# Performance work log

Hardware: AMD Instinct MI355X
Metric: run time of the kernel (lower is better)

## Reference

```python
import jax, jax.numpy as jnp
import numpy as np

N_GROUPS = 32
EPS = 1e-5
N_HEADS = 8
D_K = 64


def setup_inputs() -> dict:
    key = jax.random.key(0)
    ks = jax.random.split(key, 4)
    B, C, H, W = 16, 512, 32, 32
    x = jax.random.normal(ks[0], (B, C, H, W), dtype=jnp.float32)
    gn_w = jnp.ones((C,), dtype=jnp.float32)
    gn_b = jnp.zeros((C,), dtype=jnp.float32)
    proj_w = jax.random.normal(ks[1], (3 * C, C), dtype=jnp.float32) * (C ** -0.5)
    proj_b = jnp.zeros((3 * C,), dtype=jnp.float32)
    out_w = jax.random.normal(ks[2], (C, C), dtype=jnp.float32) * (C ** -0.5)
    out_b = jnp.zeros((C,), dtype=jnp.float32)
    return {"x": x, "gn_w": gn_w, "gn_b": gn_b, "proj_w": proj_w,
            "proj_b": proj_b, "out_w": out_w, "out_b": out_b}


def _group_norm(x, w, b):
    B, C, H, W = x.shape
    xg = x.reshape(B, N_GROUPS, C // N_GROUPS, H, W)
    mean = xg.mean(axis=(2, 3, 4), keepdims=True)
    var = xg.var(axis=(2, 3, 4), keepdims=True)
    xn = (xg - mean) * jax.lax.rsqrt(var + EPS)
    xn = xn.reshape(B, C, H, W)
    return xn * w[None, :, None, None] + b[None, :, None, None]


def reference(x, gn_w, gn_b, proj_w, proj_b, out_w, out_b):
    B, C, H, W = x.shape
    S = H * W
    scale = D_K ** -0.25  # applied to both q and k, as in the original
    h = _group_norm(x, gn_w, gn_b).reshape(B, C, S).transpose(0, 2, 1)  # [B,S,C]
    qkv = h @ proj_w.T + proj_b  # [B,S,3C]
    qkv = qkv.reshape(B, S, N_HEADS, 3 * D_K)
    q, k, v = jnp.split(qkv, 3, axis=-1)  # each [B,S,H,D]
    attn = jnp.einsum('bihd,bjhd->bijh', q * scale, k * scale)  # [B,S,S,Hd]
    attn = jax.nn.softmax(attn, axis=2)
    res = jnp.einsum('bijh,bjhd->bihd', attn, v).reshape(B, S, N_HEADS * D_K)
    res = res @ out_w.T + out_b  # [B,S,C]
    res = res.transpose(0, 2, 1).reshape(B, C, H, W)
    return res + x
```

## Files before the change

kernel.cpp:

```cpp
#include <hip/hip_runtime.h>
#include <stdint.h>

typedef unsigned short u16;
typedef __attribute__((ext_vector_type(8))) short bf16x8;
typedef __attribute__((ext_vector_type(4))) short bf16x4;
typedef __attribute__((ext_vector_type(4))) float f32x4;
typedef __attribute__((ext_vector_type(4))) unsigned short u16x4;

__device__ __forceinline__ u16 f2b(float f) {
  union { float f; unsigned u; } v; v.f = f;
  unsigned r = v.u + 0x7FFFu + ((v.u >> 16) & 1u);
  return (u16)(r >> 16);
}

__device__ __forceinline__ float fexp2(float x) {
#if __has_builtin(__builtin_amdgcn_exp2f)
  return __builtin_amdgcn_exp2f(x);
#else
  return exp2f(x);
#endif
}

__global__ __launch_bounds__(256) void cvt_kernel(const float* __restrict__ wq_f,
                                                  const float* __restrict__ wo_f,
                                                  u16* __restrict__ wq,
                                                  u16* __restrict__ wo) {
  int i = blockIdx.x * 256 + threadIdx.x;
  const float* src; u16* dst; int j;
  if (i < 196608) { src = wq_f; dst = wq; j = i; }
  else            { src = wo_f; dst = wo; j = i - 196608; }
  const float4 f = ((const float4*)src)[j];
  u16x4 r; r[0] = f2b(f.x); r[1] = f2b(f.y); r[2] = f2b(f.z); r[3] = f2b(f.w);
  *(u16x4*)(dst + (size_t)j * 4) = r;
}

__global__ __launch_bounds__(256) void gn_kernel(const float* __restrict__ x,
                                                 const float* __restrict__ gw,
                                                 const float* __restrict__ gb,
                                                 u16* __restrict__ h) {
  const int b = blockIdx.x >> 5, g = blockIdx.x & 31;
  const float* xg = x + ((size_t)(b * 512 + g * 16)) * 1024;
  const int tid = threadIdx.x;
  float vals[64];
  float s = 0.f, ss = 0.f;
#pragma unroll
  for (int i = 0; i < 64; i++) {
    float vv = xg[i * 256 + tid];
    vals[i] = vv; s += vv; ss += vv * vv;
  }
#pragma unroll
  for (int off = 32; off; off >>= 1) { s += __shfl_down(s, off); ss += __shfl_down(ss, off); }
  __shared__ float red[8];
  const int wid = tid >> 6, lane = tid & 63;
  if (lane == 0) { red[wid] = s; red[4 + wid] = ss; }
  __syncthreads();
  if (tid == 0) {
    float S = red[0] + red[1] + red[2] + red[3];
    float SS = red[4] + red[5] + red[6] + red[7];
    float mean = S * (1.f / 16384.f);
    float var = SS * (1.f / 16384.f) - mean * mean;
    red[0] = mean; red[1] = rsqrtf(var + 1e-5f);
  }
  __syncthreads();
  const float mean = red[0], rs = red[1];
  float sc[16], bi[16];
#pragma unroll
  for (int c = 0; c < 16; c++) { sc[c] = gw[g * 16 + c] * rs; bi[c] = gb[g * 16 + c]; }
#pragma unroll
  for (int h4 = 0; h4 < 4; h4++) {
    const int sp = h4 * 256 + tid;
    u16 row[16];
#pragma unroll
    for (int c = 0; c < 16; c++)
      row[c] = f2b((vals[c * 4 + h4] - mean) * sc[c] + bi[c]);
    u16* dst = h + ((size_t)(b * 1024 + sp)) * 512 + g * 16;
    *(bf16x8*)dst = *(bf16x8*)&row[0];
    *(bf16x8*)(dst + 8) = *(bf16x8*)&row[8];
  }
}

#define TSTRIDE 36

__global__ __launch_bounds__(256) void qkv_gemm(const u16* __restrict__ h,
                                                const u16* __restrict__ w,
                                                const float* __restrict__ bias,
                                                u16* __restrict__ q,
                                                u16* __restrict__ k,
                                                u16* __restrict__ v) {
  __shared__ u16 As[2][128 * TSTRIDE];
  __shared__ u16 Bs[2][128 * TSTRIDE];
  const int b = blockIdx.z;
  const int bm = blockIdx.x;
  const int bn = blockIdx.y;
  const int tid = threadIdx.x, lane = tid & 63, wid = tid >> 6;
  const int wm = wid & 1, wn = wid >> 1;
  const u16* gA = h + ((size_t)b * 1024 + bm * 128) * 512;
  const u16* gB = w + (size_t)bn * 128 * 512;

  const f32x4 fz = {0.f, 0.f, 0.f, 0.f};
  f32x4 acc[4][4];
#pragma unroll
  for (int i = 0; i < 4; i++)
#pragma unroll
    for (int j = 0; j < 4; j++) acc[i][j] = fz;

  int srow[2], soff[2];
#pragma unroll
  for (int j = 0; j < 2; j++) {
    srow[j] = (wid * 2 + j) * 16 + (lane >> 2);
    soff[j] = srow[j] * TSTRIDE + (lane & 3) * 8;
  }
  const int ch8 = (lane & 3) * 8;
  const int c15 = lane & 15, quad = lane >> 4;

  bf16x8 ar[2], br[2];
#pragma unroll
  for (int j = 0; j < 2; j++) {
    ar[j] = *(const bf16x8*)(gA + (size_t)srow[j] * 512 + ch8);
    br[j] = *(const bf16x8*)(gB + (size_t)srow[j] * 512 + ch8);
  }
#pragma unroll
  for (int j = 0; j < 2; j++) {
    *(bf16x8*)&As[0][soff[j]] = ar[j];
    *(bf16x8*)&Bs[0][soff[j]] = br[j];
  }
#pragma unroll
  for (int j = 0; j < 2; j++) {
    ar[j] = *(const bf16x8*)(gA + (size_t)srow[j] * 512 + 32 + ch8);
    br[j] = *(const bf16x8*)(gB + (size_t)srow[j] * 512 + 32 + ch8);
  }

  for (int kt = 0; kt < 16; ++kt) {
    __syncthreads();
    const int cur = kt & 1, alt = cur ^ 1;
    if (kt < 15) {
#pragma unroll
      for (int j = 0; j < 2; j++) {
        *(bf16x8*)&As[alt][soff[j]] = ar[j];
        *(bf16x8*)&Bs[alt][soff[j]] = br[j];
      }
      const int pk2 = (kt + 2) & 15;
#pragma unroll
      for (int j = 0; j < 2; j++) {
        ar[j] = *(const bf16x8*)(gA + (size_t)srow[j] * 512 + pk2 * 32 + ch8);
        br[j] = *(const bf16x8*)(gB + (size_t)srow[j] * 512 + pk2 * 32 + ch8);
      }
    }
    bf16x8 af[4], bf[4];
#pragma unroll
    for (int mi = 0; mi < 4; mi++)
      af[mi] = *(const bf16x8*)&As[cur][(wm * 64 + mi * 16 + c15) * TSTRIDE + quad * 8];
#pragma unroll
    for (int ni = 0; ni < 4; ni++)
      bf[ni] = *(const bf16x8*)&Bs[cur][(wn * 64 + ni * 16 + c15) * TSTRIDE + quad * 8];
#pragma unroll
    for (int mi = 0; mi < 4; mi++)
#pragma unroll
      for (int ni = 0; ni < 4; ni++)
        acc[mi][ni] = __builtin_amdgcn_mfma_f32_16x16x32_bf16(af[mi], bf[ni], acc[mi][ni], 0, 0, 0);
  }

  const float qscale = 0.51006972f;
  const float kscale = 0.35355339059327373f;
  const int quad4 = quad << 2;
#pragma unroll
  for (int mi = 0; mi < 4; mi++) {
    const int m = bm * 128 + wm * 64 + mi * 16 + quad4;
#pragma unroll
    for (int ni = 0; ni < 4; ni++) {
      const int n = bn * 128 + wn * 64 + ni * 16 + c15;
      const int head = n / 192;
      const int rr = n - head * 192;
      const float bi = bias[n];
      const int d = rr & 63;
      if (rr < 128) {
        u16* dst = (rr < 64) ? q : k;
        const float sc = (rr < 64) ? qscale : kscale;
        dst += ((size_t)(b * 8 + head) * 1024 + m) * 64 + d;
#pragma unroll
        for (int r = 0; r < 4; r++)
          dst[(size_t)r * 64] = f2b((acc[mi][ni][r] + bi) * sc);
      } else {
        u16x4 pk;
#pragma unroll
        for (int r = 0; r < 4; r++) pk[r] = f2b(acc[mi][ni][r] + bi);
        *(u16x4*)(v + ((size_t)(b * 8 + head) * 64 + d) * 1024 + m) = pk;
      }
    }
  }
}

__global__ __launch_bounds__(256) void attn_kernel(const u16* __restrict__ q,
                                                   const u16* __restrict__ k,
                                                   const u16* __restrict__ vT,
                                                   u16* __restrict__ o) {
  __shared__ u16 Ks[2][64 * 64];
  __shared__ u16 Vs[2][64 * 64];
  const int bh = blockIdx.x;
  const int qb = blockIdx.y;
  const int tid = threadIdx.x, lane = tid & 63, wid = tid >> 6;
  const u16* Q = q + (size_t)bh * 1024 * 64;
  const u16* K = k + (size_t)bh * 1024 * 64;
  const u16* V = vT + (size_t)bh * 64 * 1024;
  const int qrow0 = qb * 128 + wid * 32;
  const int c15 = lane & 15, quad = lane >> 4;
  const int sw = c15 & 7;
  const int srow = tid >> 2;
  const int t4 = tid & 3;
  const int s7 = srow & 7;
  const int kld0 = srow * 64 + (((t4 * 2) ^ s7) * 8);
  const int kld1 = srow * 64 + (((t4 * 2 + 1) ^ s7) * 8);
  int vld[4];
#pragma unroll
  for (int qq = 0; qq < 4; qq++)
    vld[qq] = srow * 64 + ((((t4 >> 1) * 4 + qq) ^ s7) * 8) + (t4 & 1) * 4;

  bf16x8 qf[2][2];
#pragma unroll
  for (int kk = 0; kk < 2; kk++)
#pragma unroll
    for (int ni = 0; ni < 2; ni++)
      qf[kk][ni] = *(const bf16x8*)(Q + (size_t)(qrow0 + ni * 16 + c15) * 64 + kk * 32 + quad * 8);

  const f32x4 fz = {0.f, 0.f, 0.f, 0.f};
  const float Mshift = 14.4269504089f;
  const f32x4 fm = {-Mshift, -Mshift, -Mshift, -Mshift};
  f32x4 oaccT[4][2];
#pragma unroll
  for (int i = 0; i < 4; i++)
#pragma unroll
    for (int j = 0; j < 2; j++) oaccT[i][j] = fz;
  float lsum[2] = {0.f, 0.f};

  bf16x8 kr0, kr1, vr0, vr1;
  {
    const u16* Kn = K + (size_t)srow * 64 + t4 * 16;
    kr0 = *(const bf16x8*)(Kn); kr1 = *(const bf16x8*)(Kn + 8);
    const u16* Vn = V + (size_t)srow * 1024 + t4 * 16;
    vr0 = *(const bf16x8*)(Vn); vr1 = *(const bf16x8*)(Vn + 8);
  }
  {
    u16* Kd = Ks[0]; u16* Vd = Vs[0];
    *(bf16x8*)&Kd[kld0] = kr0; *(bf16x8*)&Kd[kld1] = kr1;
    union { bf16x4 h[2]; bf16x8 v; } a0, a1;
    a0.v = vr0; a1.v = vr1;
    *(bf16x4*)&Vd[vld[0]] = a0.h[0];
    *(bf16x4*)&Vd[vld[1]] = a0.h[1];
    *(bf16x4*)&Vd[vld[2]] = a1.h[0];
    *(bf16x4*)&Vd[vld[3]] = a1.h[1];
  }
  {
    const u16* Kn = K + (size_t)(64 + srow) * 64 + t4 * 16;
    kr0 = *(const bf16x8*)(Kn); kr1 = *(const bf16x8*)(Kn + 8);
    const u16* Vn = V + (size_t)srow * 1024 + 64 + t4 * 16;
    vr0 = *(const bf16x8*)(Vn); vr1 = *(const bf16x8*)(Vn + 8);
  }

  for (int kt = 0; kt < 16; ++kt) {
    __syncthreads();
    const int cur = kt & 1, alt = cur ^ 1;
    if (kt < 15) {
      u16* Kd = Ks[alt]; u16* Vd = Vs[alt];
      *(bf16x8*)&Kd[kld0] = kr0; *(bf16x8*)&Kd[kld1] = kr1;
      union { bf16x4 h[2]; bf16x8 v; } a0, a1;
      a0.v = vr0; a1.v = vr1;
      *(bf16x4*)&Vd[vld[0]] = a0.h[0];
      *(bf16x4*)&Vd[vld[1]] = a0.h[1];
      *(bf16x4*)&Vd[vld[2]] = a1.h[0];
      *(bf16x4*)&Vd[vld[3]] = a1.h[1];
      const int pk2 = (kt + 2) & 15;
      const u16* Kn = K + ((size_t)pk2 * 64 + srow) * 64 + t4 * 16;
      kr0 = *(const bf16x8*)(Kn); kr1 = *(const bf16x8*)(Kn + 8);
      const u16* Vn = V + (size_t)srow * 1024 + pk2 * 64 + t4 * 16;
      vr0 = *(const bf16x8*)(Vn); vr1 = *(const bf16x8*)(Vn + 8);
    }
    const u16* Kc = Ks[cur];
    const u16* Vc = Vs[cur];

    f32x4 sacc[4][2];
#pragma unroll
    for (int i = 0; i < 4; i++)
#pragma unroll
      for (int j = 0; j < 2; j++) sacc[i][j] = fm;
#pragma unroll
    for (int kk = 0; kk < 2; kk++) {
      bf16x8 af[4];
#pragma unroll
      for (int mi = 0; mi < 4; mi++)
        af[mi] = *(const bf16x8*)&Kc[(mi * 16 + c15) * 64 + (((kk * 4 + quad) ^ sw) * 8)];
#pragma unroll
      for (int mi = 0; mi < 4; mi++)
#pragma unroll
        for (int ni = 0; ni < 2; ni++)
          sacc[mi][ni] = __builtin_amdgcn_mfma_f32_16x16x32_bf16(af[mi], qf[kk][ni], sacc[mi][ni], 0, 0, 0);
    }

    unsigned pkd[4][2][2];
#pragma unroll
    for (int ni = 0; ni < 2; ni++) {
      float ls = 0.f;
#pragma unroll
      for (int mi = 0; mi < 4; mi++) {
        unsigned pu[4];
#pragma unroll
        for (int r = 0; r < 4; r++) {
          const float p = fexp2(sacc[mi][ni][r]);
          ls += p;
          union { float f; unsigned u; } c; c.f = p;
          pu[r] = c.u;
        }
        pkd[mi][ni][0] = __builtin_amdgcn_perm(pu[1], pu[0], 0x07060302u);
        pkd[mi][ni][1] = __builtin_amdgcn_perm(pu[3], pu[2], 0x07060302u);
      }
      lsum[ni] += ls;
    }

#pragma unroll
    for (int mg = 0; mg < 2; mg++) {
      union { unsigned u[4]; bf16x8 v; } bb[2];
#pragma unroll
      for (int ni = 0; ni < 2; ni++) {
        bb[ni].u[0] = pkd[2 * mg][ni][0];     bb[ni].u[1] = pkd[2 * mg][ni][1];
        bb[ni].u[2] = pkd[2 * mg + 1][ni][0]; bb[ni].u[3] = pkd[2 * mg + 1][ni][1];
      }
#pragma unroll
      for (int nd = 0; nd < 4; nd++) {
        const bf16x8 aa = *(const bf16x8*)&Vc[(nd * 16 + c15) * 64 + (((mg * 4 + quad) ^ sw) * 8)];
#pragma unroll
        for (int ni = 0; ni < 2; ni++)
          oaccT[nd][ni] = __builtin_amdgcn_mfma_f32_16x16x32_bf16(aa, bb[ni].v, oaccT[nd][ni], 0, 0, 0);
      }
    }
  }

  float iv[2];
#pragma unroll
  for (int ni = 0; ni < 2; ni++) {
    float l = lsum[ni];
    l += __shfl_xor(l, 16);
    l += __shfl_xor(l, 32);
    iv[ni] = 1.f / l;
  }
  const int b = bh >> 3, hh = bh & 7;
#pragma unroll
  for (int ni = 0; ni < 2; ni++) {
    const int row = qrow0 + ni * 16 + c15;
#pragma unroll
    for (int nd = 0; nd < 4; nd++) {
      u16x4 pk4;
#pragma unroll
      for (int r = 0; r < 4; r++) pk4[r] = f2b(oaccT[nd][ni][r] * iv[ni]);
      *(u16x4*)(o + ((size_t)b * 1024 + row) * 512 + hh * 64 + nd * 16 + quad * 4) = pk4;
    }
  }
}

__global__ __launch_bounds__(256) void out_gemm(const u16* __restrict__ wo,
                                                const u16* __restrict__ attn,
                                                const float* __restrict__ ob,
                                                const float* __restrict__ x,
                                                float* __restrict__ out) {
  __shared__ u16 As[2][128 * TSTRIDE];
  __shared__ u16 Bs[2][128 * TSTRIDE];
  const int b = blockIdx.z;
  const int bm = blockIdx.x;
  const int bn = blockIdx.y;
  const int tid = threadIdx.x, lane = tid & 63, wid = tid >> 6;
  const int wm = wid & 1, wn = wid >> 1;
  const u16* gA = wo + (size_t)bm * 128 * 512;
  const u16* gB = attn + ((size_t)b * 1024 + bn * 128) * 512;

  const f32x4 fz = {0.f, 0.f, 0.f, 0.f};
  f32x4 acc[4][4];
#pragma unroll
  for (int i = 0; i < 4; i++)
#pragma unroll
    for (int j = 0; j < 4; j++) acc[i][j] = fz;

  int srow[2], soff[2];
#pragma unroll
  for (int j = 0; j < 2; j++) {
    srow[j] = (wid * 2 + j) * 16 + (lane >> 2);
    soff[j] = srow[j] * TSTRIDE + (lane & 3) * 8;
  }
  const int ch8 = (lane & 3) * 8;
  const int c15 = lane & 15, quad = lane >> 4;

  bf16x8 ar[2], br[2];
#pragma unroll
  for (int j = 0; j < 2; j++) {
    ar[j] = *(const bf16x8*)(gA + (size_t)srow[j] * 512 + ch8);
    br[j] = *(const bf16x8*)(gB + (size_t)srow[j] * 512 + ch8);
  }
#pragma unroll
  for (int j = 0; j < 2; j++) {
    *(bf16x8*)&As[0][soff[j]] = ar[j];
    *(bf16x8*)&Bs[0][soff[j]] = br[j];
  }
#pragma unroll
  for (int j = 0; j < 2; j++) {
    ar[j] = *(const bf16x8*)(gA + (size_t)srow[j] * 512 + 32 + ch8);
    br[j] = *(const bf16x8*)(gB + (size_t)srow[j] * 512 + 32 + ch8);
  }

  for (int kt = 0; kt < 16; ++kt) {
    __syncthreads();
    const int cur = kt & 1, alt = cur ^ 1;
    if (kt < 15) {
#pragma unroll
      for (int j = 0; j < 2; j++) {
        *(bf16x8*)&As[alt][soff[j]] = ar[j];
        *(bf16x8*)&Bs[alt][soff[j]] = br[j];
      }
      const int pk2 = (kt + 2) & 15;
#pragma unroll
      for (int j = 0; j < 2; j++) {
        ar[j] = *(const bf16x8*)(gA + (size_t)srow[j] * 512 + pk2 * 32 + ch8);
        br[j] = *(const bf16x8*)(gB + (size_t)srow[j] * 512 + pk2 * 32 + ch8);
      }
    }
    bf16x8 af[4], bf[4];
#pragma unroll
    for (int mi = 0; mi < 4; mi++)
      af[mi] = *(const bf16x8*)&As[cur][(wm * 64 + mi * 16 + c15) * TSTRIDE + quad * 8];
#pragma unroll
    for (int ni = 0; ni < 4; ni++)
      bf[ni] = *(const bf16x8*)&Bs[cur][(wn * 64 + ni * 16 + c15) * TSTRIDE + quad * 8];
#pragma unroll
    for (int mi = 0; mi < 4; mi++)
#pragma unroll
      for (int ni = 0; ni < 4; ni++)
        acc[mi][ni] = __builtin_amdgcn_mfma_f32_16x16x32_bf16(af[mi], bf[ni], acc[mi][ni], 0, 0, 0);
  }

  const int quad4 = quad << 2;
#pragma unroll
  for (int mi = 0; mi < 4; mi++) {
    const int c = bm * 128 + wm * 64 + mi * 16 + quad4;
#pragma unroll
    for (int ni = 0; ni < 4; ni++) {
      const int s = bn * 128 + wn * 64 + ni * 16 + c15;
#pragma unroll
      for (int r = 0; r < 4; r++) {
        const int cc = c + r;
        const size_t idx = ((size_t)b * 512 + cc) * 1024 + s;
        out[idx] = acc[mi][ni][r] + ob[cc] + x[idx];
      }
    }
  }
}

extern "C" void kernel_launch(void* const* d_in, const int* in_sizes, int n_in,
                              void* d_out, int out_size, void* d_ws, size_t ws_size,
                              hipStream_t stream) {
  const float* x      = (const float*)d_in[0];
  const float* gn_w   = (const float*)d_in[1];
  const float* gn_b   = (const float*)d_in[2];
  const float* proj_w = (const float*)d_in[3];
  const float* proj_b = (const float*)d_in[4];
  const float* out_w  = (const float*)d_in[5];
  const float* out_b  = (const float*)d_in[6];
  float* out = (float*)d_out;

  char* p = (char*)d_ws;
  u16* h    = (u16*)p; p += (size_t)16 * 1024 * 512 * 2;
  u16* q    = (u16*)p; p += (size_t)16 * 8 * 1024 * 64 * 2;
  u16* k    = (u16*)p; p += (size_t)16 * 8 * 1024 * 64 * 2;
  u16* v    = (u16*)p; p += (size_t)16 * 8 * 1024 * 64 * 2;
  u16* attn = (u16*)p; p += (size_t)16 * 1024 * 512 * 2;
  u16* wq   = (u16*)p; p += (size_t)1536 * 512 * 2;
  u16* wo   = (u16*)p; p += (size_t)512 * 512 * 2;

  cvt_kernel<<<1024, 256, 0, stream>>>(proj_w, out_w, wq, wo);
  gn_kernel<<<512, 256, 0, stream>>>(x, gn_w, gn_b, h);
  qkv_gemm<<<dim3(8, 12, 16), 256, 0, stream>>>(h, wq, proj_b, q, k, v);
  attn_kernel<<<dim3(128, 8, 1), 256, 0, stream>>>(q, k, v, attn);
  out_gemm<<<dim3(4, 8, 16), 256, 0, stream>>>(wo, attn, out_b, x, out);
}
```

Measured before the change: 219.9 us.

## Double query rows per attention block to reuse K/V tiles across more queries

Each wave now handles 64 query rows instead of 32, processed as two 32-row halves per key tile, and the grid's query dimension is halved. V fragments are loaded from shared memory once per tile and reused for both halves. This halves the global K/V loads and LDS staging per query and amortizes the V fragment reads. In exchange it raises register use (more accumulators and query fragments) and halves the number of blocks, which can reduce occupancy.

Result: no change. 216.6 us (-1.5%).

```diff
diff --git a/kernel.cpp b/kernel.cpp
--- a/kernel.cpp
+++ b/kernel.cpp
@@ -202,7 +202,7 @@
   const u16* Q = q + (size_t)bh * 1024 * 64;
   const u16* K = k + (size_t)bh * 1024 * 64;
   const u16* V = vT + (size_t)bh * 64 * 1024;
-  const int qrow0 = qb * 128 + wid * 32;
+  const int qrow0 = qb * 256 + wid * 64;
   const int c15 = lane & 15, quad = lane >> 4;
   const int sw = c15 & 7;
   const int srow = tid >> 2;
@@ -215,22 +215,22 @@
   for (int qq = 0; qq < 4; qq++)
     vld[qq] = srow * 64 + ((((t4 >> 1) * 4 + qq) ^ s7) * 8) + (t4 & 1) * 4;
 
-  bf16x8 qf[2][2];
+  bf16x8 qf[2][4];
 #pragma unroll
   for (int kk = 0; kk < 2; kk++)
 #pragma unroll
-    for (int ni = 0; ni < 2; ni++)
+    for (int ni = 0; ni < 4; ni++)
       qf[kk][ni] = *(const bf16x8*)(Q + (size_t)(qrow0 + ni * 16 + c15) * 64 + kk * 32 + quad * 8);
 
   const f32x4 fz = {0.f, 0.f, 0.f, 0.f};
   const float Mshift = 14.4269504089f;
   const f32x4 fm = {-Mshift, -Mshift, -Mshift, -Mshift};
-  f32x4 oaccT[4][2];
+  f32x4 oaccT[4][4];
 #pragma unroll
   for (int i = 0; i < 4; i++)
 #pragma unroll
-    for (int j = 0; j < 2; j++) oaccT[i][j] = fz;
-  float lsum[2] = {0.f, 0.f};
+    for (int j = 0; j < 4; j++) oaccT[i][j] = fz;
+  float lsum[4] = {0.f, 0.f, 0.f, 0.f};
 
   bf16x8 kr0, kr1, vr0, vr1;
   {
@@ -277,65 +277,73 @@
     const u16* Kc = Ks[cur];
     const u16* Vc = Vs[cur];
 
-    f32x4 sacc[4][2];
-#pragma unroll
-    for (int i = 0; i < 4; i++)
-#pragma unroll
-      for (int j = 0; j < 2; j++) sacc[i][j] = fm;
-#pragma unroll
-    for (int kk = 0; kk < 2; kk++) {
-      bf16x8 af[4];
-#pragma unroll
-      for (int mi = 0; mi < 4; mi++)
-        af[mi] = *(const bf16x8*)&Kc[(mi * 16 + c15) * 64 + (((kk * 4 + quad) ^ sw) * 8)];
-#pragma unroll
-      for (int mi = 0; mi < 4; mi++)
-#pragma unroll
-        for (int ni = 0; ni < 2; ni++)
-          sacc[mi][ni] = __builtin_amdgcn_mfma_f32_16x16x32_bf16(af[mi], qf[kk][ni], sacc[mi][ni], 0, 0, 0);
-    }
-
-    unsigned pkd[4][2][2];
-#pragma unroll
-    for (int ni = 0; ni < 2; ni++) {
-      float ls = 0.f;
-#pragma unroll
-      for (int mi = 0; mi < 4; mi++) {
-        unsigned pu[4];
-#pragma unroll
-        for (int r = 0; r < 4; r++) {
-          const float p = fexp2(sacc[mi][ni][r]);
-          ls += p;
-          union { float f; unsigned u; } c; c.f = p;
-          pu[r] = c.u;
+    bf16x8 vfr[2][4];
+#pragma unroll
+    for (int mg = 0; mg < 2; mg++)
+#pragma unroll
+      for (int nd = 0; nd < 4; nd++)
+        vfr[mg][nd] = *(const bf16x8*)&Vc[(nd * 16 + c15) * 64 + (((mg * 4 + quad) ^ sw) * 8)];
+
+#pragma unroll
+    for (int p = 0; p < 2; p++) {
+      f32x4 sacc[4][2];
+#pragma unroll
+      for (int i = 0; i < 4; i++)
+#pragma unroll
+        for (int j = 0; j < 2; j++) sacc[i][j] = fm;
+#pragma unroll
+      for (int kk = 0; kk < 2; kk++) {
+        bf16x8 af[4];
+#pragma unroll
+        for (int mi = 0; mi < 4; mi++)
+          af[mi] = *(const bf16x8*)&Kc[(mi * 16 + c15) * 64 + (((kk * 4 + quad) ^ sw) * 8)];
+#pragma unroll
+        for (int mi = 0; mi < 4; mi++)
+#pragma unroll
+          for (int nj = 0; nj < 2; nj++)
+            sacc[mi][nj] = __builtin_amdgcn_mfma_f32_16x16x32_bf16(af[mi], qf[kk][2 * p + nj], sacc[mi][nj], 0, 0, 0);
+      }
+
+      unsigned pkd[4][2][2];
+#pragma unroll
+      for (int nj = 0; nj < 2; nj++) {
+        float ls = 0.f;
+#pragma unroll
+        for (int mi = 0; mi < 4; mi++) {
+          unsigned pu[4];
+#pragma unroll
+          for (int r = 0; r < 4; r++) {
+            const float pp = fexp2(sacc[mi][nj][r]);
+            ls += pp;
+            union { float f; unsigned u; } c; c.f = pp;
+            pu[r] = c.u;
+          }
+          pkd[mi][nj][0] = __builtin_amdgcn_perm(pu[1], pu[0], 0x07060302u);
+          pkd[mi][nj][1] = __builtin_amdgcn_perm(pu[3], pu[2], 0x07060302u);
         }
-        pkd[mi][ni][0] = __builtin_amdgcn_perm(pu[1], pu[0], 0x07060302u);
-        pkd[mi][ni][1] = __builtin_amdgcn_perm(pu[3], pu[2], 0x07060302u);
-      }
-      lsum[ni] += ls;
-    }
-
-#pragma unroll
-    for (int mg = 0; mg < 2; mg++) {
-      union { unsigned u[4]; bf16x8 v; } bb[2];
-#pragma unroll
-      for (int ni = 0; ni < 2; ni++) {
-        bb[ni].u[0] = pkd[2 * mg][ni][0];     bb[ni].u[1] = pkd[2 * mg][ni][1];
-        bb[ni].u[2] = pkd[2 * mg + 1][ni][0]; bb[ni].u[3] = pkd[2 * mg + 1][ni][1];
-      }
-#pragma unroll
-      for (int nd = 0; nd < 4; nd++) {
-        const bf16x8 aa = *(const bf16x8*)&Vc[(nd * 16 + c15) * 64 + (((mg * 4 + quad) ^ sw) * 8)];
-#pragma unroll
-        for (int ni = 0; ni < 2; ni++)
-          oaccT[nd][ni] = __builtin_amdgcn_mfma_f32_16x16x32_bf16(aa, bb[ni].v, oaccT[nd][ni], 0, 0, 0);
-      }
-    }
-  }
-
-  float iv[2];
-#pragma unroll
-  for (int ni = 0; ni < 2; ni++) {
+        lsum[2 * p + nj] += ls;
+      }
+
+#pragma unroll
+      for (int mg = 0; mg < 2; mg++) {
+        union { unsigned u[4]; bf16x8 v; } bb[2];
+#pragma unroll
+        for (int nj = 0; nj < 2; nj++) {
+          bb[nj].u[0] = pkd[2 * mg][nj][0];     bb[nj].u[1] = pkd[2 * mg][nj][1];
+          bb[nj].u[2] = pkd[2 * mg + 1][nj][0]; bb[nj].u[3] = pkd[2 * mg + 1][nj][1];
+        }
+#pragma unroll
+        for (int nd = 0; nd < 4; nd++)
+#pragma unroll
+          for (int nj = 0; nj < 2; nj++)
+            oaccT[nd][2 * p + nj] = __builtin_amdgcn_mfma_f32_16x16x32_bf16(vfr[mg][nd], bb[nj].v, oaccT[nd][2 * p + nj], 0, 0, 0);
+      }
+    }
+  }
+
+  float iv[4];
+#pragma unroll
+  for (int ni = 0; ni < 4; ni++) {
     float l = lsum[ni];
     l += __shfl_xor(l, 16);
     l += __shfl_xor(l, 32);
@@ -343,7 +351,7 @@
   }
   const int b = bh >> 3, hh = bh & 7;
 #pragma unroll
-  for (int ni = 0; ni < 2; ni++) {
+  for (int ni = 0; ni < 4; ni++) {
     const int row = qrow0 + ni * 16 + c15;
 #pragma unroll
     for (int nd = 0; nd < 4; nd++) {
@@ -474,6 +482,6 @@
   cvt_kernel<<<1024, 256, 0, stream>>>(proj_w, out_w, wq, wo);
   gn_kernel<<<512, 256, 0, stream>>>(x, gn_w, gn_b, h);
   qkv_gemm<<<dim3(8, 12, 16), 256, 0, stream>>>(h, wq, proj_b, q, k, v);
-  attn_kernel<<<dim3(128, 8, 1), 256, 0, stream>>>(q, k, v, attn);
+  attn_kernel<<<dim3(128, 4, 1), 256, 0, stream>>>(q, k, v, attn);
   out_gemm<<<dim3(4, 8, 16), 256, 0, stream>>>(wo, attn, out_b, x, out);
 }
```
